# Kernel tuning notes

Hardware: AMD Instinct MI355X
Metric: run time of the kernel (lower is better)

The kernel has to match this reference:

```python
import jax, jax.numpy as jnp
import numpy as np

NEG = -1e9  # finite stand-in for -inf (keeps gradients NaN-free)
BLANK_LOGPROB = -1.0


def _lse(*xs):
    m = xs[0]
    for x in xs[1:]:
        m = jnp.maximum(m, x)
    s = sum(jnp.exp(x - m) for x in xs)
    return m + jnp.log(s)


def _forward_sum_loss(attn_logprob, text_lens, mel_lens):
    # attn_logprob: [B, 1, T, U]; text/mel lens: [B] int
    B, _, T, U = attn_logprob.shape
    x = attn_logprob[:, 0]                                   # [B, T, U]
    # pad a blank column at text index 0 (F.pad(..., (1,0,...)), value=blank_logprob)
    x = jnp.pad(x, ((0, 0), (0, 0), (1, 0)), constant_values=BLANK_LOGPROB)  # [B,T,U+1]
    # per-sample log_softmax over only the first text_len+1 columns (matches the
    # torch slice [:, :, :text_len+1] before LogSoftmax) -> mask padding columns
    cols = jnp.arange(U + 1)
    valid_col = cols[None, :] <= text_lens[:, None]          # [B, U+1]
    x = jnp.where(valid_col[:, None, :], x, NEG)
    lp = jax.nn.log_softmax(x, axis=-1)                      # [B, T, U+1]

    # CTC forward-sum. Target for sample b is [1, 2, ..., text_len_b] (all
    # distinct labels), extended with blanks: s=0..2U, label(s)=0 if s even else (s+1)//2.
    S = 2 * U + 1
    s = jnp.arange(S)
    lab = jnp.where(s % 2 == 0, 0, (s + 1) // 2)             # [S]
    odd = (s % 2 == 1)
    lp_ext = lp[:, :, lab]                                   # [B, T, S]
    # columns beyond text_len are NEG after log_softmax, so invalid label
    # positions (odd s with (s+1)//2 > text_len) are automatically killed.

    idx_last = 2 * text_lens                                 # [B] final blank position
    neg1 = jnp.full((B, 1), NEG, lp.dtype)
    neg2 = jnp.full((B, 2), NEG, lp.dtype)

    def step(alpha, lp_t):
        a1 = alpha                                           # stay
        a2 = jnp.concatenate([neg1, alpha[:, :-1]], axis=1)  # advance 1
        a3 = jnp.concatenate([neg2, alpha[:, :-2]], axis=1)  # skip (labels distinct)
        a3 = jnp.where(odd[None, :], a3, NEG)                # skip only into label positions
        new = lp_t + _lse(a1, a2, a3)                        # [B, S]
        fin = _lse(jnp.take_along_axis(new, idx_last[:, None], axis=1)[:, 0],
                   jnp.take_along_axis(new, (idx_last - 1)[:, None], axis=1)[:, 0])
        return new, fin

    alpha0 = jnp.full((B, S), NEG, lp.dtype).at[:, 0].set(0.0)
    lp_ts = jnp.transpose(lp_ext, (1, 0, 2))                 # [T, B, S]
    _, fins = jax.lax.scan(step, alpha0, lp_ts)              # [T, B]
    final = jnp.take_along_axis(fins, (mel_lens - 1)[None, :], axis=0)[0]  # [B]
    # nn.CTCLoss(reduction='mean') on a batch of 1 divides by target length;
    # zero_infinity zeroes out impossible alignments.
    loss = jnp.where(final < NEG / 2, 0.0, -final / text_lens.astype(lp.dtype))
    return jnp.mean(loss)


def setup_inputs() -> dict:
    key = jax.random.key(0)
    k1, k2, k3 = jax.random.split(key, 3)
    B, T, U = 64, 1000, 250
    attn_logprob = jax.random.normal(k1, (B, 1, T, U), dtype=jnp.float32)
    text_lens = jax.random.randint(k2, (B,), 50, U + 1, dtype=jnp.int32)
    mel_lens = jax.random.randint(k3, (B,), 600, T + 1, dtype=jnp.int32)
    return {"attn_logprob": attn_logprob, "text_lens": text_lens, "mel_lens": mel_lens}


def reference(attn_logprob, text_lens, mel_lens):
    return _forward_sum_loss(attn_logprob, text_lens, mel_lens)
```

## Files before the change

### kernel.cpp

```cpp
#include <hip/hip_runtime.h>

#define NEGF -1000000000.0f
#define LOG2E 1.4426950408889634f
#define LN2 0.6931471805599453f

constexpr int Bn = 64;
constexpr int Tn = 1000;
constexpr int Un = 250;

__device__ __forceinline__ float exp2fast(float x) { return __builtin_amdgcn_exp2f(x); }
__device__ __forceinline__ float log2fast(float x) { return __builtin_amdgcn_logf(x); }

template <int CTRL>
__device__ __forceinline__ float dppmov(float x) {
    return __int_as_float(__builtin_amdgcn_update_dpp(
        0, __float_as_int(x), CTRL, 0xf, 0xf, true));
}
__device__ __forceinline__ float wave_red_max(float x) {
    x = fmaxf(x, dppmov<0x111>(x));
    x = fmaxf(x, dppmov<0x112>(x));
    x = fmaxf(x, dppmov<0x114>(x));
    x = fmaxf(x, dppmov<0x118>(x));
    x = fmaxf(x, dppmov<0x142>(x));
    x = fmaxf(x, dppmov<0x143>(x));
    return __int_as_float(__builtin_amdgcn_readlane(__float_as_int(x), 63));
}
__device__ __forceinline__ float wave_red_sum(float x) {
    x += dppmov<0x111>(x);
    x += dppmov<0x112>(x);
    x += dppmov<0x114>(x);
    x += dppmov<0x118>(x);
    x += dppmov<0x142>(x);
    x += dppmov<0x143>(x);
    return __int_as_float(__builtin_amdgcn_readlane(__float_as_int(x), 63));
}

__global__ void __launch_bounds__(256) zrow_kernel(const float* __restrict__ attn,
                                                   const int* __restrict__ text_lens,
                                                   float* __restrict__ Z2) {
    int wid = threadIdx.x >> 6;
    int lane = threadIdx.x & 63;
    int row = blockIdx.x * 4 + wid;
    if (row >= Bn * Tn) return;
    int b = row / Tn;
    int L = text_lens[b];
    const float* p = attn + (size_t)row * Un;

    float v[4];
    float m = (lane == 0) ? -LOG2E : NEGF;
#pragma unroll
    for (int i = 0; i < 4; ++i) {
        int u = lane + 64 * i;
        v[i] = (u < L) ? p[u] * LOG2E : NEGF;
        m = fmaxf(m, v[i]);
    }
    m = wave_red_max(m);
    float s = (lane == 0) ? exp2fast(-LOG2E - m) : 0.0f;
#pragma unroll
    for (int i = 0; i < 4; ++i) s += exp2fast(v[i] - m);
    s = wave_red_sum(s);
    if (lane == 0) Z2[row] = m + log2fast(s);
}

typedef float v2f __attribute__((ext_vector_type(2)));

#define CTC_REFILL(J, T)                                                      \
    {                                                                         \
        int tl_ = (T) <= last ? (T) : last;                                   \
        const char* rowp_ = pbase + (size_t)tl_ * 1000;                       \
        asm volatile("global_load_dwordx2 %0, %1, %2"                         \
                     : "=v"(lo[J]) : "v"(voff_lo), "s"(rowp_));               \
        asm volatile("global_load_dwordx2 %0, %1, %2"                         \
                     : "=v"(hi[J]) : "v"(voff_hi), "s"(rowp_));               \
    }

#define CTC_STEP(J, WCNT)                                                     \
    {                                                                         \
        asm volatile("s_waitcnt vmcnt(" #WCNT ")"                             \
                     : "+v"(lo[J]), "+v"(hi[J]));                             \
        float q0 = exp2fast(__builtin_fmaf(lo[J].x, LOG2E, bias0));           \
        float q1 = exp2fast(__builtin_fmaf(lo[J].y, LOG2E, bias1));           \
        float q2 = exp2fast(__builtin_fmaf(hi[J].x, LOG2E, bias2));           \
        float q3 = exp2fast(__builtin_fmaf(hi[J].y, LOG2E, bias3));           \
        float s65 = a6 + a5, s43 = a4 + a3, s21 = a2 + a1;                    \
        float na7 = (a7 + s65) * q3;                                          \
        float t7 = __shfl_up(na7, 1);          \
        a6 = s65 * QB;                                                        \
        a5 = (a5 + s43) * q2;                                                 \
        a4 = s43 * QB;                                                        \
        a3 = (a3 + s21) * q1;                                                 \
        a2 = s21 * QB;                                                        \
        float s0p = a0 + p7c;                                                 \
        a1 = (a1 + s0p) * q0;                                                 \
        a0 = s0p * QB;                                                        \
        a7 = na7;                                                             \
        p7c = (lane == 0) ? 0.0f : t7;                                        \
    }

#define RENORM()                                                              \
    {                                                                         \
        float mx = fmaxf(fmaxf(fmaxf(a0, a1), fmaxf(a2, a3)),                 \
                         fmaxf(fmaxf(a4, a5), fmaxf(a6, a7)));                \
        mx = wave_red_max(mx);                \
        int e_ = (int)((__float_as_uint(mx) >> 23) & 255) - 127;              \
        float scale_ = __uint_as_float((unsigned)(127 - e_) << 23);           \
        a0 *= scale_; a1 *= scale_; a2 *= scale_; a3 *= scale_;               \
        a4 *= scale_; a5 *= scale_; a6 *= scale_; a7 *= scale_;               \
        p7c *= scale_;      \
        Esum += (float)e_;                                                    \
    }

__global__ void __launch_bounds__(64, 1) ctc_kernel(const float* __restrict__ attn,
                                                    const int* __restrict__ text_lens,
                                                    const int* __restrict__ mel_lens,
                                                    const float* __restrict__ Z2,
                                                    float* __restrict__ out) {
    int b = blockIdx.x;
    int lane = threadIdx.x;
    int L = text_lens[b];
    int n_t = mel_lens[b];
    const char* pbase = (const char*)(attn + (size_t)b * Tn * Un);

    int voff_lo = lane * 16, voff_hi = lane * 16 + 8;
    if (lane == 62) { voff_lo = 992; voff_hi = 992; }
    if (lane == 63) { voff_lo = 0;   voff_hi = 0;   }
    int c0 = lane * 4;
    float bias0 = (c0 + 0 < L) ? 0.0f : -1000000.0f;
    float bias1 = (c0 + 1 < L) ? 0.0f : -1000000.0f;
    float bias2 = (c0 + 2 < L) ? 0.0f : -1000000.0f;
    float bias3 = (c0 + 3 < L) ? 0.0f : -1000000.0f;

    const float QB = 0.36787944117144233f;
    float a0 = (lane == 0) ? 1.0f : 0.0f;
    float a1 = 0.0f, a2 = 0.0f, a3 = 0.0f, a4 = 0.0f, a5 = 0.0f, a6 = 0.0f, a7 = 0.0f;
    float p7c = 0.0f;
    float Esum = 0.0f;

    v2f lo[16], hi[16];
    int last = n_t - 1;

#pragma unroll
    for (int j = 0; j < 16; ++j) CTC_REFILL(j, j);

    int full = n_t & ~15;
    int t = 0;
    for (; t < full; t += 16) {
        CTC_STEP(0, 30);  CTC_REFILL(0, t + 16);
        CTC_STEP(1, 30);  CTC_REFILL(1, t + 17);
        CTC_STEP(2, 30);  CTC_REFILL(2, t + 18);
        CTC_STEP(3, 30);  CTC_REFILL(3, t + 19);
        CTC_STEP(4, 30);  CTC_REFILL(4, t + 20);
        CTC_STEP(5, 30);  CTC_REFILL(5, t + 21);
        CTC_STEP(6, 30);  CTC_REFILL(6, t + 22);
        CTC_STEP(7, 30);  CTC_REFILL(7, t + 23);
        RENORM();
        CTC_STEP(8, 30);  CTC_REFILL(8, t + 24);
        CTC_STEP(9, 30);  CTC_REFILL(9, t + 25);
        CTC_STEP(10, 30); CTC_REFILL(10, t + 26);
        CTC_STEP(11, 30); CTC_REFILL(11, t + 27);
        CTC_STEP(12, 30); CTC_REFILL(12, t + 28);
        CTC_STEP(13, 30); CTC_REFILL(13, t + 29);
        CTC_STEP(14, 30); CTC_REFILL(14, t + 30);
        CTC_STEP(15, 30); CTC_REFILL(15, t + 31);
        RENORM();
    }
    if (t + 0 < n_t) CTC_STEP(0, 0);
    if (t + 1 < n_t) CTC_STEP(1, 0);
    if (t + 2 < n_t) CTC_STEP(2, 0);
    if (t + 3 < n_t) CTC_STEP(3, 0);
    if (t + 4 < n_t) CTC_STEP(4, 0);
    if (t + 5 < n_t) CTC_STEP(5, 0);
    if (t + 6 < n_t) CTC_STEP(6, 0);
    if (t + 7 < n_t) CTC_STEP(7, 0);
    if (t + 8 < n_t) { RENORM(); CTC_STEP(8, 0); }
    if (t + 9 < n_t) CTC_STEP(9, 0);
    if (t + 10 < n_t) CTC_STEP(10, 0);
    if (t + 11 < n_t) CTC_STEP(11, 0);
    if (t + 12 < n_t) CTC_STEP(12, 0);
    if (t + 13 < n_t) CTC_STEP(13, 0);
    if (t + 14 < n_t) CTC_STEP(14, 0);
    asm volatile("s_waitcnt vmcnt(0)" ::: "memory");

    __shared__ float sal[512];
    sal[lane * 8 + 0] = a0;
    sal[lane * 8 + 1] = a1;
    sal[lane * 8 + 2] = a2;
    sal[lane * 8 + 3] = a3;
    sal[lane * 8 + 4] = a4;
    sal[lane * 8 + 5] = a5;
    sal[lane * 8 + 6] = a6;
    sal[lane * 8 + 7] = a7;
    __syncthreads();

    float zs = 0.0f;
    for (int i = lane; i < n_t; i += 64) zs += Z2[b * Tn + i];
    zs = wave_red_sum(zs);

    if (lane == 0) {
        float ssum = sal[2 * L] + sal[2 * L - 1];
        float fin = (log2fast(ssum) + Esum - zs) * LN2;
        float loss = (ssum <= 0.0f) ? 0.0f : (-fin / (float)L);
        atomicAdd(out, loss * (1.0f / (float)Bn));
    }
}

extern "C" void kernel_launch(void* const* d_in, const int* in_sizes, int n_in,
                              void* d_out, int out_size, void* d_ws, size_t ws_size,
                              hipStream_t stream) {
    const float* attn = (const float*)d_in[0];
    const int* text_lens = (const int*)d_in[1];
    const int* mel_lens = (const int*)d_in[2];
    float* out = (float*)d_out;
    float* Z2 = (float*)d_ws;

    (void)hipMemsetAsync(d_out, 0, sizeof(float), stream);
    zrow_kernel<<<(Bn * Tn + 3) / 4, 256, 0, stream>>>(attn, text_lens, Z2);
    ctc_kernel<<<Bn, 64, 0, stream>>>(attn, text_lens, mel_lens, Z2, out);
}
```

Before: 194.1 us.

## Use DPP wave shift in CTC recurrence, batch zrow rows, drop memset

The CTC step now takes the neighbour lane's a7 with a DPP wave_shr1 move of the old value, replacing the ds_bpermute-based shfl_up of the freshly computed value and the lane-0 select. This takes the cross-lane exchange off the serial critical path. The zrow kernel now has each wave process four rows, with all loads issued up front for memory-level parallelism. It also zeroes the output, which removes the separate memset launch. The out-zeroing in zrow relies on stream ordering before the atomics in the ctc kernel. The DPP shift is assumed to shift in zero at lane 0 because bound_ctrl is set.

```diff
diff --git a/kernel.cpp b/kernel.cpp
--- a/kernel.cpp
+++ b/kernel.cpp
@@ -16,6 +16,8 @@
     return __int_as_float(__builtin_amdgcn_update_dpp(
         0, __float_as_int(x), CTRL, 0xf, 0xf, true));
 }
+__device__ __forceinline__ float dpp_wave_shr1(float x) { return dppmov<0x138>(x); }
+
 __device__ __forceinline__ float wave_red_max(float x) {
     x = fmaxf(x, dppmov<0x111>(x));
     x = fmaxf(x, dppmov<0x112>(x));
@@ -37,29 +39,43 @@
 
 __global__ void __launch_bounds__(256) zrow_kernel(const float* __restrict__ attn,
                                                    const int* __restrict__ text_lens,
-                                                   float* __restrict__ Z2) {
+                                                   float* __restrict__ Z2,
+                                                   float* __restrict__ out) {
+    if (blockIdx.x == 0 && threadIdx.x == 0) *out = 0.0f;
     int wid = threadIdx.x >> 6;
     int lane = threadIdx.x & 63;
-    int row = blockIdx.x * 4 + wid;
-    if (row >= Bn * Tn) return;
-    int b = row / Tn;
-    int L = text_lens[b];
-    const float* p = attn + (size_t)row * Un;
-
-    float v[4];
-    float m = (lane == 0) ? -LOG2E : NEGF;
-#pragma unroll
-    for (int i = 0; i < 4; ++i) {
-        int u = lane + 64 * i;
-        v[i] = (u < L) ? p[u] * LOG2E : NEGF;
-        m = fmaxf(m, v[i]);
-    }
-    m = wave_red_max(m);
-    float s = (lane == 0) ? exp2fast(-LOG2E - m) : 0.0f;
-#pragma unroll
-    for (int i = 0; i < 4; ++i) s += exp2fast(v[i] - m);
-    s = wave_red_sum(s);
-    if (lane == 0) Z2[row] = m + log2fast(s);
+    int row0 = (blockIdx.x * 4 + wid) * 4;
+
+    float v[4][4];
+    int Ls[4];
+#pragma unroll
+    for (int r = 0; r < 4; ++r) {
+        int row = row0 + r;
+        Ls[r] = text_lens[row / Tn];
+        const float* p = attn + (size_t)row * Un;
+#pragma unroll
+        for (int i = 0; i < 4; ++i) {
+            int u = lane + 64 * i;
+            v[r][i] = (u < Un) ? p[u] : 0.0f;
+        }
+    }
+#pragma unroll
+    for (int r = 0; r < 4; ++r) {
+        int L = Ls[r];
+        float m = (lane == 0) ? -LOG2E : NEGF;
+#pragma unroll
+        for (int i = 0; i < 4; ++i) {
+            int u = lane + 64 * i;
+            v[r][i] = (u < L) ? v[r][i] * LOG2E : NEGF;
+            m = fmaxf(m, v[r][i]);
+        }
+        m = wave_red_max(m);
+        float s = (lane == 0) ? exp2fast(-LOG2E - m) : 0.0f;
+#pragma unroll
+        for (int i = 0; i < 4; ++i) s += exp2fast(v[r][i] - m);
+        s = wave_red_sum(s);
+        if (lane == 0) Z2[row0 + r] = m + log2fast(s);
+    }
 }
 
 typedef float v2f __attribute__((ext_vector_type(2)));
@@ -82,19 +98,12 @@
         float q1 = exp2fast(__builtin_fmaf(lo[J].y, LOG2E, bias1));           \
         float q2 = exp2fast(__builtin_fmaf(hi[J].x, LOG2E, bias2));           \
         float q3 = exp2fast(__builtin_fmaf(hi[J].y, LOG2E, bias3));           \
-        float s65 = a6 + a5, s43 = a4 + a3, s21 = a2 + a1;                    \
-        float na7 = (a7 + s65) * q3;                                          \
-        float t7 = __shfl_up(na7, 1);          \
-        a6 = s65 * QB;                                                        \
-        a5 = (a5 + s43) * q2;                                                 \
-        a4 = s43 * QB;                                                        \
-        a3 = (a3 + s21) * q1;                                                 \
-        a2 = s21 * QB;                                                        \
-        float s0p = a0 + p7c;                                                 \
-        a1 = (a1 + s0p) * q0;                                                 \
-        a0 = s0p * QB;                                                        \
-        a7 = na7;                                                             \
-        p7c = (lane == 0) ? 0.0f : t7;                                        \
+        float p7 = dpp_wave_shr1(a7);       \
+        float s65 = a6 + a5, s43 = a4 + a3, s21 = a2 + a1, s0p = a0 + p7;     \
+        a7 = (a7 + s65) * q3;  a6 = s65 * QB;                                 \
+        a5 = (a5 + s43) * q2;  a4 = s43 * QB;                                 \
+        a3 = (a3 + s21) * q1;  a2 = s21 * QB;                                 \
+        a1 = (a1 + s0p) * q0;  a0 = s0p * QB;                                 \
     }
 
 #define RENORM()                                                              \
@@ -106,7 +115,6 @@
         float scale_ = __uint_as_float((unsigned)(127 - e_) << 23);           \
         a0 *= scale_; a1 *= scale_; a2 *= scale_; a3 *= scale_;               \
         a4 *= scale_; a5 *= scale_; a6 *= scale_; a7 *= scale_;               \
-        p7c *= scale_;      \
         Esum += (float)e_;                                                    \
     }
 
@@ -133,7 +141,6 @@
     const float QB = 0.36787944117144233f;
     float a0 = (lane == 0) ? 1.0f : 0.0f;
     float a1 = 0.0f, a2 = 0.0f, a3 = 0.0f, a4 = 0.0f, a5 = 0.0f, a6 = 0.0f, a7 = 0.0f;
-    float p7c = 0.0f;
     float Esum = 0.0f;
 
     v2f lo[16], hi[16];
@@ -213,7 +220,6 @@
     float* out = (float*)d_out;
     float* Z2 = (float*)d_ws;
 
-    (void)hipMemsetAsync(d_out, 0, sizeof(float), stream);
-    zrow_kernel<<<(Bn * Tn + 3) / 4, 256, 0, stream>>>(attn, text_lens, Z2);
+    zrow_kernel<<<Bn * Tn / 16, 256, 0, stream>>>(attn, text_lens, Z2, out);
     ctc_kernel<<<Bn, 64, 0, stream>>>(attn, text_lens, mel_lens, Z2, out);
 }
```

Measured after the change: 172.5 us. 1.13x faster.
